# Kernel optimization log

Measured on AMD Instinct MI355X. Metric: run time of the kernel, lower is better.

The kernel has to match this reference:

```python
import jax, jax.numpy as jnp
from jax import lax
import numpy as np

B = 128            # graphs
N = 2048           # nodes per graph (contiguous per graph)
DEG = 8            # avg degree
E = B * N * DEG    # 2,097,152 edges
F_IN = 64
K1 = int(np.ceil(0.8 * N))    # 1639, TopKPooling ratio=0.8
K2 = int(np.ceil(0.8 * K1))   # 1312


def setup_inputs() -> dict:
    key = jax.random.key(0)
    ks = jax.random.split(key, 20)
    # within-graph random edges: global index = graph_offset + local index
    epg = N * DEG  # edges per graph
    offs = (jnp.arange(B, dtype=jnp.int64) * N)[:, None]
    src = (jax.random.randint(ks[0], (B, epg), 0, N) + offs).reshape(-1)
    dst = (jax.random.randint(ks[1], (B, epg), 0, N) + offs).reshape(-1)
    edge_index = jnp.stack([src, dst]).astype(jnp.int64)
    batch = jnp.repeat(jnp.arange(B, dtype=jnp.int64), N)
    r = lambda k, s: jax.random.normal(k, s, dtype=jnp.float32)
    return {
        "x": r(ks[2], (B * N, F_IN)),
        "edge_index": edge_index,
        "edge_attr": jax.random.uniform(ks[3], (E,), dtype=jnp.float32),
        "batch": batch,
        "W1_rel": r(ks[4], (F_IN, 32)) / np.sqrt(F_IN),
        "b1": r(ks[5], (32,)) * 0.01,
        "W1_root": r(ks[6], (F_IN, 32)) / np.sqrt(F_IN),
        "p1_w": r(ks[7], (32,)),
        "W2_rel": r(ks[8], (32, 32)) / np.sqrt(32),
        "b2": r(ks[9], (32,)) * 0.01,
        "W2_root": r(ks[10], (32, 32)) / np.sqrt(32),
        "p2_w": r(ks[11], (32,)),
        "lin1_W": r(ks[12], (64, 32)) / 8.0,
        "lin1_b": r(ks[13], (32,)) * 0.01,
        "lin2_W": r(ks[14], (32, 16)) / np.sqrt(32),
        "lin2_b": r(ks[15], (16,)) * 0.01,
        "lin3_W": r(ks[16], (16, 2)) / 4.0,
        "lin3_b": r(ks[17], (2,)) * 0.01,
    }


def _graph_conv(x, src, dst, ew, W_rel, b, W_root, num_nodes):
    # PyG GraphConv: out_i = W_rel @ sum_j w_ji x_j + W_root @ x_i + b
    msg = x[src] * ew[:, None]                                   # [E, F]
    agg = jax.ops.segment_sum(msg, dst, num_segments=num_nodes)  # [N, F]
    return agg @ W_rel + b + x @ W_root


def _topk_pool(x, pw, nodes_per_graph, k):
    # PyG TopKPooling: score = tanh((x . w)/||w||); keep top-k per graph;
    # x_out = x[perm] * score[perm]
    score = jnp.tanh((x @ pw) / jnp.linalg.norm(pw))             # [B*n]
    _, idx = lax.top_k(score.reshape(B, nodes_per_graph), k)     # [B, k] local
    perm = (idx + (jnp.arange(B) * nodes_per_graph)[:, None]).reshape(-1)
    xp = x[perm] * score[perm][:, None]                          # [B*k, F]
    return xp, perm


def reference(x, edge_index, edge_attr, batch, W1_rel, b1, W1_root, p1_w,
              W2_rel, b2, W2_root, p2_w, lin1_W, lin1_b, lin2_W, lin2_b,
              lin3_W, lin3_b):
    src, dst = edge_index[0], edge_index[1]
    n0 = B * N
    # conv1 + pool1
    h = jax.nn.relu(_graph_conv(x, src, dst, edge_attr, W1_rel, b1, W1_root, n0))
    h, perm1 = _topk_pool(h, p1_w, N, K1)                        # [B*K1, 32]
    # filter_adj: keep edges with both endpoints selected, remap indices;
    # invalid edges get weight 0 (no contribution to segment_sum)
    mapping = jnp.full((n0,), -1, dtype=jnp.int32).at[perm1].set(
        jnp.arange(B * K1, dtype=jnp.int32))
    ns, nd = mapping[src], mapping[dst]
    valid = (ns >= 0) & (nd >= 0)
    ew2 = jnp.where(valid, edge_attr, 0.0)
    src2 = jnp.where(valid, ns, 0)
    dst2 = jnp.where(valid, nd, 0)
    hb = h.reshape(B, K1, 32)
    x1 = jnp.concatenate([hb.max(axis=1), hb.mean(axis=1)], axis=1)  # [B, 64]
    # conv2 + pool2
    h = jax.nn.relu(_graph_conv(h, src2, dst2, ew2, W2_rel, b2, W2_root, B * K1))
    h, _ = _topk_pool(h, p2_w, K1, K2)                           # [B*K2, 32]
    hb = h.reshape(B, K2, 32)
    x2 = jnp.concatenate([hb.max(axis=1), hb.mean(axis=1)], axis=1)  # [B, 64]
    # readout MLP (dropout is identity in eval mode)
    z = x1 + x2
    z = jax.nn.relu(z @ lin1_W + lin1_b)
    z = jax.nn.relu(z @ lin2_W + lin2_b)
    return jax.nn.log_softmax(z @ lin3_W + lin3_b, axis=-1)      # [B, 2]
```

## Files before the change

kernel.cpp:

```cpp
#include <hip/hip_runtime.h>
#include <hip/hip_fp16.h>
#include <math.h>

#define NNODES (128*2048)
#define NEDGES (NNODES*8)
#define NPG 2048
#define EPG (NPG*8)
#define HPG (EPG/2)
#define NGRAPH 128
#define KSEL1 1639
#define KSEL2 1312

__device__ __forceinline__ unsigned packh2(float a, float b) {
    __half2 h = __floats2half2_rn(a, b);
    return *reinterpret_cast<unsigned*>(&h);
}
__device__ __forceinline__ float2 unph2(unsigned u) {
    __half2 h = *reinterpret_cast<__half2*>(&u);
    return __half22float2(h);
}
__device__ __forceinline__ unsigned wscan_u(unsigned v, int lane) {
    #pragma unroll
    for (int off = 1; off < 64; off <<= 1) {
        unsigned n = __shfl_up(v, off);
        if (lane >= off) v += n;
    }
    return v;
}
__device__ __forceinline__ int wscan_i(int v, int lane) {
    #pragma unroll
    for (int off = 1; off < 64; off <<= 1) {
        int n = __shfl_up(v, off);
        if (lane >= off) v += n;
    }
    return v;
}

__global__ __launch_bounds__(1024) void k_csr(
    const int* __restrict__ src, const int* __restrict__ dst,
    const float* __restrict__ ew, int2* __restrict__ meta,
    int2* __restrict__ edge_sorted)
{
    __shared__ int2 ebuf[HPG];
    __shared__ int cnt[NPG];
    __shared__ int curs[NPG];
    __shared__ int wpart[16];
    int t = threadIdx.x;
    int lane = t & 63, wv = t >> 6;
    int bid = blockIdx.x;
    int g = bid >> 1, part = bid & 1;
    const int ebase = g * EPG + part * HPG;
    int ds[8], ss[8]; float wws[8];
    #pragma unroll
    for (int j=0;j<8;++j) {
        int idx = ebase + t + 1024*j;
        ds[j] = dst[idx] & (NPG-1);
        ss[j] = src[idx];
        wws[j] = ew[idx];
    }
    for (int i = t; i < NPG; i += 1024) cnt[i] = 0;
    __syncthreads();
    #pragma unroll
    for (int j=0;j<8;++j) atomicAdd(&cnt[ds[j]], 1);
    __syncthreads();
    int base = t * 2;
    int l0 = cnt[base], l1 = cnt[base+1];
    int s0 = l0 + l1;
    int sc = wscan_i(s0, lane);
    if (lane == 63) wpart[wv] = sc;
    __syncthreads();
    int b = 0;
    for (int i = 0; i < wv; ++i) b += wpart[i];
    int run = b + sc - s0;
    curs[base] = run; curs[base+1] = run + l0;
    __syncthreads();
    for (int i = t; i < NPG; i += 1024)
        meta[(size_t)part*NNODES + g*NPG + i] = make_int2(ebase + curs[i], cnt[i]);
    __syncthreads();
    #pragma unroll
    for (int j=0;j<8;++j) {
        int pos = atomicAdd(&curs[ds[j]], 1);
        ebuf[pos] = make_int2(ss[j], __float_as_int(wws[j]));
    }
    __syncthreads();
    for (int i = t; i < NPG; i += 1024) {
        int cv = cnt[i];
        if (cv > 1) {
            int beg = curs[i] - cv;
            for (int a = 1; a < cv; ++a) {
                int2 key = ebuf[beg + a];
                unsigned long long kk =
                    ((unsigned long long)(unsigned)key.x << 32) | (unsigned)key.y;
                int p = beg + a - 1;
                while (p >= beg) {
                    int2 cur = ebuf[p];
                    unsigned long long ck =
                        ((unsigned long long)(unsigned)cur.x << 32) | (unsigned)cur.y;
                    if (ck <= kk) break;
                    ebuf[p + 1] = cur;
                    --p;
                }
                ebuf[p + 1] = key;
            }
        }
    }
    __syncthreads();
    #pragma unroll
    for (int j=0;j<8;++j) {
        int i = t + 1024*j;
        edge_sorted[ebase + i] = ebuf[i];
    }
}

#define XP 36
__global__ __launch_bounds__(256, 4) void k_gemm64(
    const float* __restrict__ x, const float* __restrict__ Wrel,
    const float* __restrict__ Wroot, const float* __restrict__ b,
    unsigned char* __restrict__ yb, unsigned char* __restrict__ seedb)
{
    __shared__ float xs[128*XP];
    __shared__ float wcat[64*64];
    __shared__ float bb[32];
    int t = threadIdx.x;
    for (int i = t; i < 64*64; i += 256) {
        int k = i >> 6, j = i & 63;
        wcat[i] = (j < 32) ? Wrel[k*32 + j] : Wroot[k*32 + (j-32)];
    }
    if (t < 32) bb[t] = b[t];
    size_t nb = (size_t)blockIdx.x * 128;
    int q = t >> 5, ng = t & 31;
    float acc[4][8];
    #pragma unroll
    for (int i=0;i<4;++i)
        #pragma unroll
        for (int j=0;j<8;++j) acc[i][j]=0.f;
    for (int half = 0; half < 2; ++half) {
        __syncthreads();
        const float* xg = x + nb*64 + half*32;
        for (int i = t; i < 128*8; i += 256) {
            int r = i >> 3, c = i & 7;
            *(float4*)(&xs[r*XP + c*4]) = *(const float4*)(xg + r*64 + c*4);
        }
        __syncthreads();
        int kb = half*32;
        #pragma unroll 2
        for (int k = 0; k < 32; k += 4) {
            float4 w0[4], w1[4];
            #pragma unroll
            for (int kk=0;kk<4;++kk) {
                w0[kk] = *(const float4*)(&wcat[(kb+k+kk)*64 + q*8]);
                w1[kk] = *(const float4*)(&wcat[(kb+k+kk)*64 + q*8 + 4]);
            }
            #pragma unroll
            for (int i=0;i<4;++i) {
                float4 xv = *(const float4*)(&xs[(ng + i*32)*XP + k]);
                float xvv[4] = {xv.x, xv.y, xv.z, xv.w};
                #pragma unroll
                for (int kk=0;kk<4;++kk) {
                    acc[i][0]=fmaf(xvv[kk], w0[kk].x, acc[i][0]);
                    acc[i][1]=fmaf(xvv[kk], w0[kk].y, acc[i][1]);
                    acc[i][2]=fmaf(xvv[kk], w0[kk].z, acc[i][2]);
                    acc[i][3]=fmaf(xvv[kk], w0[kk].w, acc[i][3]);
                    acc[i][4]=fmaf(xvv[kk], w1[kk].x, acc[i][4]);
                    acc[i][5]=fmaf(xvv[kk], w1[kk].y, acc[i][5]);
                    acc[i][6]=fmaf(xvv[kk], w1[kk].z, acc[i][6]);
                    acc[i][7]=fmaf(xvv[kk], w1[kk].w, acc[i][7]);
                }
            }
        }
    }
    if (q < 4) {
        #pragma unroll
        for (int i=0;i<4;++i) {
            uint4 pk;
            pk.x = packh2(acc[i][0], acc[i][1]);
            pk.y = packh2(acc[i][2], acc[i][3]);
            pk.z = packh2(acc[i][4], acc[i][5]);
            pk.w = packh2(acc[i][6], acc[i][7]);
            *(uint4*)(yb + (nb + ng + i*32)*64 + q*16) = pk;
        }
    } else {
        int qq = q - 4;
        float b0=bb[qq*8+0],b1=bb[qq*8+1],b2=bb[qq*8+2],b3=bb[qq*8+3];
        float b4=bb[qq*8+4],b5=bb[qq*8+5],b6=bb[qq*8+6],b7=bb[qq*8+7];
        #pragma unroll
        for (int i=0;i<4;++i) {
            uint4 pk;
            pk.x = packh2(acc[i][0]+b0, acc[i][1]+b1);
            pk.y = packh2(acc[i][2]+b2, acc[i][3]+b3);
            pk.z = packh2(acc[i][4]+b4, acc[i][5]+b5);
            pk.w = packh2(acc[i][6]+b6, acc[i][7]+b7);
            *(uint4*)(seedb + (nb + ng + i*32)*64 + qq*16) = pk;
        }
    }
}

__global__ __launch_bounds__(256, 4) void k_gemm32(
    const unsigned char* __restrict__ hb, const float* __restrict__ ts,
    const float* __restrict__ Wrel, const float* __restrict__ Wroot,
    const float* __restrict__ b, unsigned char* __restrict__ yb,
    unsigned char* __restrict__ seedb)
{
    __shared__ float xs[128*XP];
    __shared__ float wcat[32*64];
    __shared__ float bb[32];
    int t = threadIdx.x;
    for (int i = t; i < 32*64; i += 256) {
        int k = i >> 6, j = i & 63;
        wcat[i] = (j < 32) ? Wrel[k*32 + j] : Wroot[k*32 + (j-32)];
    }
    if (t < 32) bb[t] = b[t];
    size_t nb = (size_t)blockIdx.x * 128;
    const unsigned char* hg = hb + nb * 64;
    for (int i = t; i < 128*4; i += 256) {
        int r = i >> 2, c = i & 3;
        uint4 u = *(const uint4*)(hg + r*64 + c*16);
        float2 p0=unph2(u.x), p1=unph2(u.y), p2=unph2(u.z), p3=unph2(u.w);
        float* dst = &xs[r*XP + c*8];
        *(float4*)(dst)   = make_float4(p0.x,p0.y,p1.x,p1.y);
        *(float4*)(dst+4) = make_float4(p2.x,p2.y,p3.x,p3.y);
    }
    __syncthreads();
    int q = t >> 5, ng = t & 31;
    float tsv[4];
    #pragma unroll
    for (int i=0;i<4;++i) tsv[i] = ts[nb + ng + i*32];
    float acc[4][8];
    #pragma unroll
    for (int i=0;i<4;++i)
        #pragma unroll
        for (int j=0;j<8;++j) acc[i][j]=0.f;
    #pragma unroll 2
    for (int k = 0; k < 32; k += 4) {
        float4 w0[4], w1[4];
        #pragma unroll
        for (int kk=0;kk<4;++kk) {
            w0[kk] = *(const float4*)(&wcat[(k+kk)*64 + q*8]);
            w1[kk] = *(const float4*)(&wcat[(k+kk)*64 + q*8 + 4]);
        }
        #pragma unroll
        for (int i=0;i<4;++i) {
            float4 xv = *(const float4*)(&xs[(ng + i*32)*XP + k]);
            float xvv[4] = {xv.x, xv.y, xv.z, xv.w};
            #pragma unroll
            for (int kk=0;kk<4;++kk) {
                acc[i][0]=fmaf(xvv[kk], w0[kk].x, acc[i][0]);
                acc[i][1]=fmaf(xvv[kk], w0[kk].y, acc[i][1]);
                acc[i][2]=fmaf(xvv[kk], w0[kk].z, acc[i][2]);
                acc[i][3]=fmaf(xvv[kk], w0[kk].w, acc[i][3]);
                acc[i][4]=fmaf(xvv[kk], w1[kk].x, acc[i][4]);
                acc[i][5]=fmaf(xvv[kk], w1[kk].y, acc[i][5]);
                acc[i][6]=fmaf(xvv[kk], w1[kk].z, acc[i][6]);
                acc[i][7]=fmaf(xvv[kk], w1[kk].w, acc[i][7]);
            }
        }
    }
    if (q < 4) {
        #pragma unroll
        for (int i=0;i<4;++i) {
            float sc = tsv[i];
            uint4 pk;
            pk.x = packh2(acc[i][0]*sc, acc[i][1]*sc);
            pk.y = packh2(acc[i][2]*sc, acc[i][3]*sc);
            pk.z = packh2(acc[i][4]*sc, acc[i][5]*sc);
            pk.w = packh2(acc[i][6]*sc, acc[i][7]*sc);
            *(uint4*)(yb + (nb + ng + i*32)*64 + q*16) = pk;
        }
    } else {
        int qq = q - 4;
        float b0=bb[qq*8+0],b1=bb[qq*8+1],b2=bb[qq*8+2],b3=bb[qq*8+3];
        float b4=bb[qq*8+4],b5=bb[qq*8+5],b6=bb[qq*8+6],b7=bb[qq*8+7];
        #pragma unroll
        for (int i=0;i<4;++i) {
            float sc = tsv[i];
            uint4 pk;
            pk.x = packh2(acc[i][0]*sc+b0, acc[i][1]*sc+b1);
            pk.y = packh2(acc[i][2]*sc+b2, acc[i][3]*sc+b3);
            pk.z = packh2(acc[i][4]*sc+b4, acc[i][5]*sc+b5);
            pk.w = packh2(acc[i][6]*sc+b6, acc[i][7]*sc+b7);
            *(uint4*)(seedb + (nb + ng + i*32)*64 + qq*16) = pk;
        }
    }
}

__global__ __launch_bounds__(256) void k_gather(
    const int2* __restrict__ meta, const int2* __restrict__ edge_sorted,
    const unsigned char* __restrict__ yb, const float* __restrict__ pw,
    const int* __restrict__ mask, const unsigned char* __restrict__ seedb,
    unsigned char* __restrict__ hout, float* __restrict__ s)
{
    unsigned orig = blockIdx.x;
    unsigned nwg8 = gridDim.x >> 3;
    unsigned bid = (orig & 7u) * nwg8 + (orig >> 3);
    size_t tid = (size_t)bid * 256 + threadIdx.x;
    int node = (int)(tid >> 2);
    int q = (int)(tid & 3);
    float4 wv0 = ((const float4*)pw)[2*q];
    float4 wv1 = ((const float4*)pw)[2*q+1];
    float nn = wv0.x*wv0.x + wv0.y*wv0.y + wv0.z*wv0.z + wv0.w*wv0.w
             + wv1.x*wv1.x + wv1.y*wv1.y + wv1.z*wv1.z + wv1.w*wv1.w;
    nn += __shfl_xor(nn, 1); nn += __shfl_xor(nn, 2);
    float nrm = sqrtf(nn);
    bool valid = mask ? (mask[node] != 0) : true;
    float4 a0 = make_float4(0.f,0.f,0.f,0.f), a1 = make_float4(0.f,0.f,0.f,0.f);
    float4 b0 = make_float4(0.f,0.f,0.f,0.f), b1 = make_float4(0.f,0.f,0.f,0.f);
    if (valid) {
        uint4 su = *(const uint4*)(seedb + (size_t)node * 64 + q * 16);
        float2 s0 = unph2(su.x), s1 = unph2(su.y), s2 = unph2(su.z), s3 = unph2(su.w);
        a0 = make_float4(s0.x, s0.y, s1.x, s1.y);
        a1 = make_float4(s2.x, s2.y, s3.x, s3.y);
        #pragma unroll
        for (int p = 0; p < 2; ++p) {
            int2 m = meta[(size_t)p*NNODES + node];
            int e = m.x, end = m.x + m.y;
            for (; e + 1 < end; e += 2) {
                int2 ed0 = edge_sorted[e];
                int2 ed1 = edge_sorted[e+1];
                uint4 u0 = *(const uint4*)(yb + (size_t)ed0.x * 64 + q * 16);
                uint4 u1 = *(const uint4*)(yb + (size_t)ed1.x * 64 + q * 16);
                float w0 = __int_as_float(ed0.y);
                float w1 = __int_as_float(ed1.y);
                float2 p0, p1;
                p0 = unph2(u0.x); p1 = unph2(u0.y);
                a0.x = fmaf(p0.x, w0, a0.x); a0.y = fmaf(p0.y, w0, a0.y);
                a0.z = fmaf(p1.x, w0, a0.z); a0.w = fmaf(p1.y, w0, a0.w);
                p0 = unph2(u0.z); p1 = unph2(u0.w);
                a1.x = fmaf(p0.x, w0, a1.x); a1.y = fmaf(p0.y, w0, a1.y);
                a1.z = fmaf(p1.x, w0, a1.z); a1.w = fmaf(p1.y, w0, a1.w);
                p0 = unph2(u1.x); p1 = unph2(u1.y);
                b0.x = fmaf(p0.x, w1, b0.x); b0.y = fmaf(p0.y, w1, b0.y);
                b0.z = fmaf(p1.x, w1, b0.z); b0.w = fmaf(p1.y, w1, b0.w);
                p0 = unph2(u1.z); p1 = unph2(u1.w);
                b1.x = fmaf(p0.x, w1, b1.x); b1.y = fmaf(p0.y, w1, b1.y);
                b1.z = fmaf(p1.x, w1, b1.z); b1.w = fmaf(p1.y, w1, b1.w);
            }
            if (e < end) {
                int2 ed0 = edge_sorted[e];
                uint4 u0 = *(const uint4*)(yb + (size_t)ed0.x * 64 + q * 16);
                float w0 = __int_as_float(ed0.y);
                float2 p0, p1;
                p0 = unph2(u0.x); p1 = unph2(u0.y);
                a0.x = fmaf(p0.x, w0, a0.x); a0.y = fmaf(p0.y, w0, a0.y);
                a0.z = fmaf(p1.x, w0, a0.z); a0.w = fmaf(p1.y, w0, a0.w);
                p0 = unph2(u0.z); p1 = unph2(u0.w);
                a1.x = fmaf(p0.x, w0, a1.x); a1.y = fmaf(p0.y, w0, a1.y);
                a1.z = fmaf(p1.x, w0, a1.z); a1.w = fmaf(p1.y, w0, a1.w);
            }
        }
    }
    float hv0x = fmaxf(a0.x + b0.x, 0.f), hv0y = fmaxf(a0.y + b0.y, 0.f);
    float hv0z = fmaxf(a0.z + b0.z, 0.f), hv0w = fmaxf(a0.w + b0.w, 0.f);
    float hv1x = fmaxf(a1.x + b1.x, 0.f), hv1y = fmaxf(a1.y + b1.y, 0.f);
    float hv1z = fmaxf(a1.z + b1.z, 0.f), hv1w = fmaxf(a1.w + b1.w, 0.f);
    uint4 hw;
    hw.x = packh2(hv0x, hv0y);
    hw.y = packh2(hv0z, hv0w);
    hw.z = packh2(hv1x, hv1y);
    hw.w = packh2(hv1z, hv1w);
    *(uint4*)(hout + (size_t)node * 64 + q * 16) = hw;
    float dot = hv0x*wv0.x + hv0y*wv0.y + hv0z*wv0.z + hv0w*wv0.w
              + hv1x*wv1.x + hv1y*wv1.y + hv1z*wv1.z + hv1w*wv1.w;
    dot += __shfl_xor(dot, 1); dot += __shfl_xor(dot, 2);
    if (q == 0) s[node] = valid ? (dot / nrm) : -INFINITY;
}

__global__ __launch_bounds__(1024) void k_pool(
    const float* __restrict__ s, const unsigned char* __restrict__ hb,
    float* __restrict__ ts_out, int* __restrict__ mask_out,
    float* __restrict__ xout, int ksel)
{
    __shared__ unsigned keys[NPG];
    __shared__ unsigned hist[256];
    __shared__ unsigned wpart[16];
    __shared__ unsigned char flag[NPG];
    __shared__ unsigned sh_bin, sh_krem;
    __shared__ float red[16*64];
    int t = threadIdx.x;
    int g = blockIdx.x;
    int lane = t & 63, wv = t >> 6;
    const float* sg = s + (size_t)g * NPG;
    for (int i = t; i < NPG; i += 1024) {
        unsigned u = __float_as_uint(sg[i]);
        keys[i] = (u & 0x80000000u) ? ~u : (u | 0x80000000u);
    }
    __syncthreads();
    unsigned prefix = 0u;
    unsigned krem = (unsigned)ksel;
    for (int level = 0; level < 4; ++level) {
        int shift = 24 - 8*level;
        if (t < 256) hist[t] = 0u;
        __syncthreads();
        unsigned pmask = level ? (0xFFFFFFFFu << (shift + 8)) : 0u;
        for (int i = t; i < NPG; i += 1024) {
            unsigned key = keys[i];
            if ((key & pmask) == prefix)
                atomicAdd(&hist[(key >> shift) & 0xFFu], 1u);
        }
        __syncthreads();
        unsigned vv = 0, sc = 0;
        if (t < 256) {
            vv = hist[255 - t];
            sc = wscan_u(vv, lane);
            if (lane == 63) wpart[wv] = sc;
        }
        __syncthreads();
        if (t < 256) {
            unsigned bsum = 0;
            for (int i = 0; i < wv; ++i) bsum += wpart[i];
            unsigned incl = bsum + sc;
            unsigned excl = incl - vv;
            if (incl >= krem && excl < krem) {
                sh_bin = (unsigned)(255 - t);
                sh_krem = krem - excl;
            }
        }
        __syncthreads();
        prefix |= (sh_bin << shift);
        krem = sh_krem;
    }
    __syncthreads();
    unsigned T = prefix;
    unsigned ties = krem;
    int base = t * 2;
    unsigned k0 = keys[base], k1 = keys[base+1];
    unsigned ceq = (k0 == T ? 1u : 0u) + (k1 == T ? 1u : 0u);
    unsigned sc2 = wscan_u(ceq, lane);
    if (lane == 63) wpart[wv] = sc2;
    __syncthreads();
    unsigned bsum2 = 0;
    for (int i = 0; i < wv; ++i) bsum2 += wpart[i];
    unsigned run = bsum2 + sc2 - ceq;
    {
        unsigned char f0, f1;
        if (k0 > T) f0 = 1;
        else if (k0 == T) { f0 = (run < ties) ? 1 : 0; run++; }
        else f0 = 0;
        if (k1 > T) f1 = 1;
        else if (k1 == T) { f1 = (run < ties) ? 1 : 0; run++; }
        else f1 = 0;
        flag[base] = f0; flag[base+1] = f1;
    }
    __syncthreads();

    float mx[32], sm[32];
    #pragma unroll
    for (int j=0;j<32;++j){ mx[j]=-INFINITY; sm[j]=0.f; }
    const unsigned char* hg = hb + (size_t)g * NPG * 64;
    for (int i = t; i < NPG; i += 1024) {
        bool sel = flag[i] != 0;
        float tsv = sel ? tanhf(sg[i]) : 0.f;
        const uint4* hr = (const uint4*)(hg + (size_t)i*64);
        #pragma unroll
        for (int c4=0;c4<4;++c4) {
            uint4 u = hr[c4];
            float2 p0=unph2(u.x), p1=unph2(u.y), p2=unph2(u.z), p3=unph2(u.w);
            float vals[8] = {p0.x,p0.y,p1.x,p1.y,p2.x,p2.y,p3.x,p3.y};
            #pragma unroll
            for (int j=0;j<8;++j) {
                float v = vals[j]*tsv;
                if (sel) { mx[c4*8+j]=fmaxf(mx[c4*8+j],v); sm[c4*8+j]+=v; }
            }
        }
        if (ts_out) ts_out[(size_t)g*NPG + i] = tsv;
        if (mask_out) mask_out[(size_t)g*NPG + i] = sel ? 1 : 0;
    }
    #pragma unroll
    for (int j=0;j<32;++j) {
        for (int off=32; off; off>>=1) {
            mx[j] = fmaxf(mx[j], __shfl_xor(mx[j], off));
            sm[j] += __shfl_xor(sm[j], off);
        }
    }
    if (lane == 0) {
        #pragma unroll
        for (int j=0;j<32;++j) { red[wv*64 + j] = mx[j]; red[wv*64 + 32 + j] = sm[j]; }
    }
    __syncthreads();
    if (t < 32) {
        float m = red[t], ss = red[32 + t];
        #pragma unroll
        for (int w=1; w<16; ++w) { m = fmaxf(m, red[w*64 + t]); ss += red[w*64 + 32 + t]; }
        xout[(size_t)g*64 + t] = m;
        xout[(size_t)g*64 + 32 + t] = ss / (float)ksel;
    }
}

__global__ __launch_bounds__(128) void k_readout(
    const float* __restrict__ x1, const float* __restrict__ x2,
    const float* __restrict__ l1W, const float* __restrict__ l1b,
    const float* __restrict__ l2W, const float* __restrict__ l2b,
    const float* __restrict__ l3W, const float* __restrict__ l3b,
    float* __restrict__ out)
{
    int g = threadIdx.x;
    float z[64];
    #pragma unroll
    for (int i=0;i<64;++i) z[i] = x1[g*64+i] + x2[g*64+i];
    float a1[32];
    for (int j=0;j<32;++j) {
        float acc = l1b[j];
        #pragma unroll
        for (int i=0;i<64;++i) acc = fmaf(z[i], l1W[i*32+j], acc);
        a1[j] = fmaxf(acc, 0.f);
    }
    float a2[16];
    for (int j=0;j<16;++j) {
        float acc = l2b[j];
        #pragma unroll
        for (int i=0;i<32;++i) acc = fmaf(a1[i], l2W[i*16+j], acc);
        a2[j] = fmaxf(acc, 0.f);
    }
    float o0 = l3b[0], o1 = l3b[1];
    #pragma unroll
    for (int i=0;i<16;++i) { o0 = fmaf(a2[i], l3W[i*2+0], o0); o1 = fmaf(a2[i], l3W[i*2+1], o1); }
    float m = fmaxf(o0, o1);
    float lse = m + logf(expf(o0-m) + expf(o1-m));
    out[g*2+0] = o0 - lse;
    out[g*2+1] = o1 - lse;
}

extern "C" void kernel_launch(void* const* d_in, const int* in_sizes, int n_in,
                              void* d_out, int out_size, void* d_ws, size_t ws_size,
                              hipStream_t stream)
{
    const float* x      = (const float*)d_in[0];
    const int*   ei     = (const int*)d_in[1];
    const float* eattr  = (const float*)d_in[2];
    const float* W1rel  = (const float*)d_in[4];
    const float* b1     = (const float*)d_in[5];
    const float* W1root = (const float*)d_in[6];
    const float* p1w    = (const float*)d_in[7];
    const float* W2rel  = (const float*)d_in[8];
    const float* b2     = (const float*)d_in[9];
    const float* W2root = (const float*)d_in[10];
    const float* p2w    = (const float*)d_in[11];
    const float* l1W    = (const float*)d_in[12];
    const float* l1b    = (const float*)d_in[13];
    const float* l2W    = (const float*)d_in[14];
    const float* l2b    = (const float*)d_in[15];
    const float* l3W    = (const float*)d_in[16];
    const float* l3b    = (const float*)d_in[17];
    const int* srcp = ei;
    const int* dstp = ei + NEDGES;

    unsigned char* yb    = (unsigned char*)d_ws;
    unsigned char* seedb = yb + (size_t)NNODES*64;
    unsigned char* hb    = seedb + (size_t)NNODES*64;
    float* s1   = (float*)(hb + (size_t)NNODES*64);
    float* ts   = s1 + NNODES;
    int*   mask = (int*)(ts + NNODES);
    float* x1   = (float*)(mask + NNODES);
    float* x2   = x1 + NGRAPH*64;
    int2*  meta = (int2*)(x2 + NGRAPH*64);
    int2*  edge_sorted = (int2*)(meta + 2*NNODES);
    float* out  = (float*)d_out;

    dim3 b256(256);
    k_csr<<<NGRAPH*2, dim3(1024), 0, stream>>>(srcp, dstp, eattr, meta,
                                               edge_sorted);
    k_gemm64<<<NNODES/128, b256, 0, stream>>>(x, W1rel, W1root, b1, yb, seedb);
    k_gather<<<NNODES*4/256, b256, 0, stream>>>(meta, edge_sorted,
                                                yb, p1w, nullptr, seedb, hb, s1);
    k_pool<<<NGRAPH, dim3(1024), 0, stream>>>(s1, hb, ts, mask, x1, KSEL1);
    k_gemm32<<<NNODES/128, b256, 0, stream>>>(hb, ts, W2rel, W2root, b2, yb, seedb);
    k_gather<<<NNODES*4/256, b256, 0, stream>>>(meta, edge_sorted,
                                                yb, p2w, mask, seedb, hb, s1);
    k_pool<<<NGRAPH, dim3(1024), 0, stream>>>(s1, hb, nullptr, nullptr, x2, KSEL2);
    k_readout<<<1, 128, 0, stream>>>(x1, x2, l1W, l1b, l2W, l2b, l3W, l3b, out);
}
```

Measured before the change: 211.0 us.

## Use packed fp16 dot2 instructions in the dense GraphConv GEMM kernels

New measurement: 204.7 us. -3.0%, faster.

```diff
diff --git a/kernel.cpp b/kernel.cpp
--- a/kernel.cpp
+++ b/kernel.cpp
@@ -11,6 +11,8 @@
 #define KSEL1 1639
 #define KSEL2 1312
 
+typedef _Float16 half2_t __attribute__((ext_vector_type(2)));
+
 __device__ __forceinline__ unsigned packh2(float a, float b) {
     __half2 h = __floats2half2_rn(a, b);
     return *reinterpret_cast<unsigned*>(&h);
@@ -18,6 +20,16 @@
 __device__ __forceinline__ float2 unph2(unsigned u) {
     __half2 h = *reinterpret_cast<__half2*>(&u);
     return __half22float2(h);
+}
+__device__ __forceinline__ float fdot2u(unsigned a, unsigned b, float c) {
+#if __has_builtin(__builtin_amdgcn_fdot2)
+    half2_t ha = *reinterpret_cast<half2_t*>(&a);
+    half2_t hb = *reinterpret_cast<half2_t*>(&b);
+    return __builtin_amdgcn_fdot2(ha, hb, c, false);
+#else
+    float2 fa = unph2(a), fb = unph2(b);
+    return fmaf(fa.y, fb.y, fmaf(fa.x, fb.x, c));
+#endif
 }
 __device__ __forceinline__ unsigned wscan_u(unsigned v, int lane) {
     #pragma unroll
@@ -112,61 +124,68 @@
     }
 }
 
-#define XP 36
+#define XHP 34
 __global__ __launch_bounds__(256, 4) void k_gemm64(
     const float* __restrict__ x, const float* __restrict__ Wrel,
     const float* __restrict__ Wroot, const float* __restrict__ b,
     unsigned char* __restrict__ yb, unsigned char* __restrict__ seedb)
 {
-    __shared__ float xs[128*XP];
-    __shared__ float wcat[64*64];
+    __shared__ unsigned xh[128*XHP];
+    __shared__ unsigned wh[32*64];
     __shared__ float bb[32];
     int t = threadIdx.x;
-    for (int i = t; i < 64*64; i += 256) {
-        int k = i >> 6, j = i & 63;
-        wcat[i] = (j < 32) ? Wrel[k*32 + j] : Wroot[k*32 + (j-32)];
+    for (int i = t; i < 32*64; i += 256) {
+        int kp = i >> 6, j = i & 63;
+        float wa = (j < 32) ? Wrel[(2*kp)*32 + j]   : Wroot[(2*kp)*32 + (j-32)];
+        float wb = (j < 32) ? Wrel[(2*kp+1)*32 + j] : Wroot[(2*kp+1)*32 + (j-32)];
+        wh[i] = packh2(wa, wb);
     }
     if (t < 32) bb[t] = b[t];
     size_t nb = (size_t)blockIdx.x * 128;
+    {
+        const float4* xg4 = (const float4*)(x + nb*64);
+        #pragma unroll
+        for (int jj = 0; jj < 8; ++jj) {
+            int i = t + 256*jj;
+            int row = i >> 4, c = i & 15;
+            float4 v = xg4[i];
+            uint2 pk;
+            pk.x = packh2(v.x, v.y);
+            pk.y = packh2(v.z, v.w);
+            *(uint2*)(&xh[row*XHP + c*2]) = pk;
+        }
+    }
+    __syncthreads();
     int q = t >> 5, ng = t & 31;
     float acc[4][8];
     #pragma unroll
     for (int i=0;i<4;++i)
         #pragma unroll
         for (int j=0;j<8;++j) acc[i][j]=0.f;
-    for (int half = 0; half < 2; ++half) {
-        __syncthreads();
-        const float* xg = x + nb*64 + half*32;
-        for (int i = t; i < 128*8; i += 256) {
-            int r = i >> 3, c = i & 7;
-            *(float4*)(&xs[r*XP + c*4]) = *(const float4*)(xg + r*64 + c*4);
-        }
-        __syncthreads();
-        int kb = half*32;
-        #pragma unroll 2
-        for (int k = 0; k < 32; k += 4) {
-            float4 w0[4], w1[4];
-            #pragma unroll
-            for (int kk=0;kk<4;++kk) {
-                w0[kk] = *(const float4*)(&wcat[(kb+k+kk)*64 + q*8]);
-                w1[kk] = *(const float4*)(&wcat[(kb+k+kk)*64 + q*8 + 4]);
-            }
-            #pragma unroll
-            for (int i=0;i<4;++i) {
-                float4 xv = *(const float4*)(&xs[(ng + i*32)*XP + k]);
-                float xvv[4] = {xv.x, xv.y, xv.z, xv.w};
-                #pragma unroll
-                for (int kk=0;kk<4;++kk) {
-                    acc[i][0]=fmaf(xvv[kk], w0[kk].x, acc[i][0]);
-                    acc[i][1]=fmaf(xvv[kk], w0[kk].y, acc[i][1]);
-                    acc[i][2]=fmaf(xvv[kk], w0[kk].z, acc[i][2]);
-                    acc[i][3]=fmaf(xvv[kk], w0[kk].w, acc[i][3]);
-                    acc[i][4]=fmaf(xvv[kk], w1[kk].x, acc[i][4]);
-                    acc[i][5]=fmaf(xvv[kk], w1[kk].y, acc[i][5]);
-                    acc[i][6]=fmaf(xvv[kk], w1[kk].z, acc[i][6]);
-                    acc[i][7]=fmaf(xvv[kk], w1[kk].w, acc[i][7]);
-                }
-            }
+    for (int kp = 0; kp < 32; kp += 2) {
+        uint4 wA0 = *(const uint4*)(&wh[kp*64 + q*8]);
+        uint4 wA1 = *(const uint4*)(&wh[kp*64 + q*8 + 4]);
+        uint4 wB0 = *(const uint4*)(&wh[(kp+1)*64 + q*8]);
+        uint4 wB1 = *(const uint4*)(&wh[(kp+1)*64 + q*8 + 4]);
+        #pragma unroll
+        for (int i=0;i<4;++i) {
+            uint2 xv = *(const uint2*)(&xh[(ng + i*32)*XHP + kp]);
+            acc[i][0]=fdot2u(xv.x, wA0.x, acc[i][0]);
+            acc[i][1]=fdot2u(xv.x, wA0.y, acc[i][1]);
+            acc[i][2]=fdot2u(xv.x, wA0.z, acc[i][2]);
+            acc[i][3]=fdot2u(xv.x, wA0.w, acc[i][3]);
+            acc[i][4]=fdot2u(xv.x, wA1.x, acc[i][4]);
+            acc[i][5]=fdot2u(xv.x, wA1.y, acc[i][5]);
+            acc[i][6]=fdot2u(xv.x, wA1.z, acc[i][6]);
+            acc[i][7]=fdot2u(xv.x, wA1.w, acc[i][7]);
+            acc[i][0]=fdot2u(xv.y, wB0.x, acc[i][0]);
+            acc[i][1]=fdot2u(xv.y, wB0.y, acc[i][1]);
+            acc[i][2]=fdot2u(xv.y, wB0.z, acc[i][2]);
+            acc[i][3]=fdot2u(xv.y, wB0.w, acc[i][3]);
+            acc[i][4]=fdot2u(xv.y, wB1.x, acc[i][4]);
+            acc[i][5]=fdot2u(xv.y, wB1.y, acc[i][5]);
+            acc[i][6]=fdot2u(xv.y, wB1.z, acc[i][6]);
+            acc[i][7]=fdot2u(xv.y, wB1.w, acc[i][7]);
         }
     }
     if (q < 4) {
@@ -201,24 +220,28 @@
     const float* __restrict__ b, unsigned char* __restrict__ yb,
     unsigned char* __restrict__ seedb)
 {
-    __shared__ float xs[128*XP];
-    __shared__ float wcat[32*64];
+    __shared__ unsigned xh[128*XHP];
+    __shared__ unsigned wh[16*64];
     __shared__ float bb[32];
     int t = threadIdx.x;
-    for (int i = t; i < 32*64; i += 256) {
-        int k = i >> 6, j = i & 63;
-        wcat[i] = (j < 32) ? Wrel[k*32 + j] : Wroot[k*32 + (j-32)];
+    for (int i = t; i < 16*64; i += 256) {
+        int kp = i >> 6, j = i & 63;
+        float wa = (j < 32) ? Wrel[(2*kp)*32 + j]   : Wroot[(2*kp)*32 + (j-32)];
+        float wb = (j < 32) ? Wrel[(2*kp+1)*32 + j] : Wroot[(2*kp+1)*32 + (j-32)];
+        wh[i] = packh2(wa, wb);
     }
     if (t < 32) bb[t] = b[t];
     size_t nb = (size_t)blockIdx.x * 128;
     const unsigned char* hg = hb + nb * 64;
-    for (int i = t; i < 128*4; i += 256) {
-        int r = i >> 2, c = i & 3;
-        uint4 u = *(const uint4*)(hg + r*64 + c*16);
-        float2 p0=unph2(u.x), p1=unph2(u.y), p2=unph2(u.z), p3=unph2(u.w);
-        float* dst = &xs[r*XP + c*8];
-        *(float4*)(dst)   = make_float4(p0.x,p0.y,p1.x,p1.y);
-        *(float4*)(dst+4) = make_float4(p2.x,p2.y,p3.x,p3.y);
+    #pragma unroll
+    for (int jj = 0; jj < 4; ++jj) {
+        int i = t + 256*jj;
+        int row = i >> 3, c = i & 7;
+        uint4 u = *(const uint4*)(hg + row*64 + c*16);
+        uint2 lo; lo.x = u.x; lo.y = u.y;
+        uint2 hi; hi.x = u.z; hi.y = u.w;
+        *(uint2*)(&xh[row*XHP + c*4])     = lo;
+        *(uint2*)(&xh[row*XHP + c*4 + 2]) = hi;
     }
     __syncthreads();
     int q = t >> 5, ng = t & 31;
@@ -230,29 +253,30 @@
     for (int i=0;i<4;++i)
         #pragma unroll
         for (int j=0;j<8;++j) acc[i][j]=0.f;
-    #pragma unroll 2
-    for (int k = 0; k < 32; k += 4) {
-        float4 w0[4], w1[4];
-        #pragma unroll
-        for (int kk=0;kk<4;++kk) {
-            w0[kk] = *(const float4*)(&wcat[(k+kk)*64 + q*8]);
-            w1[kk] = *(const float4*)(&wcat[(k+kk)*64 + q*8 + 4]);
-        }
+    for (int kp = 0; kp < 16; kp += 2) {
+        uint4 wA0 = *(const uint4*)(&wh[kp*64 + q*8]);
+        uint4 wA1 = *(const uint4*)(&wh[kp*64 + q*8 + 4]);
+        uint4 wB0 = *(const uint4*)(&wh[(kp+1)*64 + q*8]);
+        uint4 wB1 = *(const uint4*)(&wh[(kp+1)*64 + q*8 + 4]);
         #pragma unroll
         for (int i=0;i<4;++i) {
-            float4 xv = *(const float4*)(&xs[(ng + i*32)*XP + k]);
-            float xvv[4] = {xv.x, xv.y, xv.z, xv.w};
-            #pragma unroll
-            for (int kk=0;kk<4;++kk) {
-                acc[i][0]=fmaf(xvv[kk], w0[kk].x, acc[i][0]);
-                acc[i][1]=fmaf(xvv[kk], w0[kk].y, acc[i][1]);
-                acc[i][2]=fmaf(xvv[kk], w0[kk].z, acc[i][2]);
-                acc[i][3]=fmaf(xvv[kk], w0[kk].w, acc[i][3]);
-                acc[i][4]=fmaf(xvv[kk], w1[kk].x, acc[i][4]);
-                acc[i][5]=fmaf(xvv[kk], w1[kk].y, acc[i][5]);
-                acc[i][6]=fmaf(xvv[kk], w1[kk].z, acc[i][6]);
-                acc[i][7]=fmaf(xvv[kk], w1[kk].w, acc[i][7]);
-            }
+            uint2 xv = *(const uint2*)(&xh[(ng + i*32)*XHP + kp]);
+            acc[i][0]=fdot2u(xv.x, wA0.x, acc[i][0]);
+            acc[i][1]=fdot2u(xv.x, wA0.y, acc[i][1]);
+            acc[i][2]=fdot2u(xv.x, wA0.z, acc[i][2]);
+            acc[i][3]=fdot2u(xv.x, wA0.w, acc[i][3]);
+            acc[i][4]=fdot2u(xv.x, wA1.x, acc[i][4]);
+            acc[i][5]=fdot2u(xv.x, wA1.y, acc[i][5]);
+            acc[i][6]=fdot2u(xv.x, wA1.z, acc[i][6]);
+            acc[i][7]=fdot2u(xv.x, wA1.w, acc[i][7]);
+            acc[i][0]=fdot2u(xv.y, wB0.x, acc[i][0]);
+            acc[i][1]=fdot2u(xv.y, wB0.y, acc[i][1]);
+            acc[i][2]=fdot2u(xv.y, wB0.z, acc[i][2]);
+            acc[i][3]=fdot2u(xv.y, wB0.w, acc[i][3]);
+            acc[i][4]=fdot2u(xv.y, wB1.x, acc[i][4]);
+            acc[i][5]=fdot2u(xv.y, wB1.y, acc[i][5]);
+            acc[i][6]=fdot2u(xv.y, wB1.z, acc[i][6]);
+            acc[i][7]=fdot2u(xv.y, wB1.w, acc[i][7]);
         }
     }
     if (q < 4) {
```
